# Performance work log

Measured on AMD Instinct MI355X. Metric: run time of the kernel, lower is better.

Reference implementation:

```python
import jax, jax.numpy as jnp
import numpy as np

NUM_NODES = 1_000_000
IN_DIM, HID = 128, 256
B = 4096                 # edges per batch (src/pos/neg each B)
N2 = 3 * B               # seed nodes
FAN = 10
N1 = N2 * FAN            # hop-1 nodes
N0 = N1 * FAN            # hop-0 nodes


def setup_inputs() -> dict:
    key = jax.random.key(0)
    ks = jax.random.split(key, 16)
    g = lambda k, shp, scale: jax.random.normal(k, shp, dtype=jnp.float32) * scale
    return {
        "node_feat": g(ks[0], (NUM_NODES, IN_DIM), 1.0),
        "gids0": jax.random.randint(ks[1], (N0,), 0, NUM_NODES, dtype=jnp.int32),
        "neigh_idx0": jax.random.randint(ks[2], (N1, FAN), 0, N0, dtype=jnp.int32),
        "neigh_idx1": jax.random.randint(ks[3], (N2, FAN), 0, N1, dtype=jnp.int32),
        "W_self0": g(ks[4], (IN_DIM, HID), (1.0 / IN_DIM) ** 0.5),
        "W_neigh0": g(ks[5], (IN_DIM, HID), (1.0 / IN_DIM) ** 0.5),
        "b0": jnp.zeros((HID,), jnp.float32),
        "W_self1": g(ks[6], (HID, HID), (1.0 / HID) ** 0.5),
        "W_neigh1": g(ks[7], (HID, HID), (1.0 / HID) ** 0.5),
        "b1": jnp.zeros((HID,), jnp.float32),
        "Wp1": g(ks[8], (HID, HID), (1.0 / HID) ** 0.5),
        "bp1": jnp.zeros((HID,), jnp.float32),
        "Wp2": g(ks[9], (HID, HID), (1.0 / HID) ** 0.5),
        "bp2": jnp.zeros((HID,), jnp.float32),
        "Wp3": g(ks[10], (HID, 1), (1.0 / HID) ** 0.5),
        "bp3": jnp.zeros((1,), jnp.float32),
    }


def _sage(x, n_dst, neigh, Ws, Wn, b):
    # x: [n_src, d]; neigh: [n_dst, fan] local indices into x
    x_dst = x[:n_dst]                       # dst nodes are a prefix of src nodes
    agg = jnp.mean(x[neigh], axis=1)        # [n_dst, d] mean aggregation
    return x_dst @ Ws + agg @ Wn + b


def reference(node_feat, gids0, neigh_idx0, neigh_idx1,
              W_self0, W_neigh0, b0, W_self1, W_neigh1, b1,
              Wp1, bp1, Wp2, bp2, Wp3, bp3):
    # embedding gather for the full sampled neighborhood
    x = node_feat[gids0]                                    # [N0, IN_DIM]
    h = jax.nn.relu(_sage(x, N1, neigh_idx0, W_self0, W_neigh0, b0))  # [N1, HID]
    h = _sage(h, N2, neigh_idx1, W_self1, W_neigh1, b1)     # [N2, HID]
    src, pos, neg = h[:B], h[B:2 * B], h[2 * B:3 * B]
    # predictor on elementwise product of endpoint embeddings
    z = jnp.concatenate([src, src], axis=0) * jnp.concatenate([pos, neg], axis=0)
    z = jax.nn.relu(z @ Wp1 + bp1)
    z = jax.nn.relu(z @ Wp2 + bp2)
    scores = z @ Wp3 + bp3                                  # [2B, 1]
    return scores
```

## Files before the change

kernel.cpp:

```cpp
#include <hip/hip_runtime.h>
#include <hip/hip_bf16.h>

#define NNODES 1000000
#define INDIM  128
#define HIDC   256
#define BSZ    4096
#define N2C    12288
#define FANC   10
#define N1C    122880
#define N0C    1228800

typedef __bf16 bf16_t;
typedef bf16_t bf16x2 __attribute__((ext_vector_type(2)));
typedef bf16_t bf16x4 __attribute__((ext_vector_type(4)));
typedef bf16_t bf16x8 __attribute__((ext_vector_type(8)));
typedef float  f32x4  __attribute__((ext_vector_type(4)));

__global__ __launch_bounds__(256) void prep_w(const float* __restrict__ SA,
                                              const float* __restrict__ SB,
                                              bf16_t* __restrict__ dst,
                                              int Khalf, int Ktot, int N) {
  int t = blockIdx.x * 256 + threadIdx.x;
  if (t >= N * Ktot) return;
  int n = t / Ktot, k = t - n * Ktot;
  float v = (k < Khalf) ? SA[(size_t)k * N + n] : SB[(size_t)(k - Khalf) * N + n];
  dst[t] = (bf16_t)v;
}

__global__ __launch_bounds__(256) void gather0(const float* __restrict__ feat,
                                               const int* __restrict__ gids,
                                               const int* __restrict__ nidx,
                                               bf16_t* __restrict__ A0) {
  int wv = (blockIdx.x * 256 + threadIdx.x) >> 6;
  int d = __builtin_amdgcn_readfirstlane(wv);
  int lane = threadIdx.x & 63;
  const float2* f2 = (const float2*)feat;
  int idx[FANC];
#pragma unroll
  for (int j = 0; j < FANC; j++) idx[j] = nidx[d * FANC + j];
  int nid[FANC];
#pragma unroll
  for (int j = 0; j < FANC; j++) nid[j] = gids[idx[j]];
  float ax = 0.f, ay = 0.f;
#pragma unroll
  for (int j = 0; j < FANC; j++) {
    float2 v = f2[(size_t)nid[j] * 64 + lane];
    ax += v.x; ay += v.y;
  }
  int sn = gids[d];
  float2 xs = f2[(size_t)sn * 64 + lane];
  bf16_t* row = A0 + (size_t)d * 256;
  bf16x2 w0 = { (bf16_t)xs.x, (bf16_t)xs.y };
  *(bf16x2*)(row + lane * 2) = w0;
  bf16x2 w1 = { (bf16_t)(ax * 0.1f), (bf16_t)(ay * 0.1f) };
  *(bf16x2*)(row + 128 + lane * 2) = w1;
}

__global__ __launch_bounds__(256) void gather1(const bf16_t* __restrict__ h,
                                               const int* __restrict__ nidx,
                                               bf16_t* __restrict__ A1) {
  int wv = (blockIdx.x * 256 + threadIdx.x) >> 6;
  int d = __builtin_amdgcn_readfirstlane(wv);
  int lane = threadIdx.x & 63;
  const bf16x4* h4 = (const bf16x4*)h;
  int idx[FANC];
#pragma unroll
  for (int j = 0; j < FANC; j++) idx[j] = nidx[d * FANC + j];
  float a0 = 0.f, a1 = 0.f, a2 = 0.f, a3 = 0.f;
#pragma unroll
  for (int j = 0; j < FANC; j++) {
    bf16x4 v = h4[(size_t)idx[j] * 64 + lane];
    a0 += (float)v[0]; a1 += (float)v[1]; a2 += (float)v[2]; a3 += (float)v[3];
  }
  bf16x4 xs = h4[(size_t)d * 64 + lane];
  bf16x4* out = (bf16x4*)(A1 + (size_t)d * 512);
  out[lane] = xs;
  bf16x4 ag = { (bf16_t)(a0 * 0.1f), (bf16_t)(a1 * 0.1f),
                (bf16_t)(a2 * 0.1f), (bf16_t)(a3 * 0.1f) };
  out[64 + lane] = ag;
}

template<int K, int MT, bool RELU, bool OUTBF>
__global__ __launch_bounds__(256) void gemm_mfma(const bf16_t* __restrict__ A,
                                                 const bf16_t* __restrict__ Wt,
                                                 const float* __restrict__ bias,
                                                 void* __restrict__ Cout) {
  int tid = threadIdx.x;
  int wv = tid >> 6, lane = tid & 63;
  int l15 = lane & 15, quad = lane >> 4;
  int m0 = blockIdx.x * (MT * 16);
  int n0 = wv * 64;
  f32x4 acc[MT][4] = {};
  for (int k0 = 0; k0 < K; k0 += 32) {
    bf16x8 a[MT], b[4];
#pragma unroll
    for (int mt = 0; mt < MT; mt++)
      a[mt] = *(const bf16x8*)(A + (size_t)(m0 + mt * 16 + l15) * K + k0 + quad * 8);
#pragma unroll
    for (int nt = 0; nt < 4; nt++)
      b[nt] = *(const bf16x8*)(Wt + (size_t)(n0 + nt * 16 + l15) * K + k0 + quad * 8);
#pragma unroll
    for (int mt = 0; mt < MT; mt++)
#pragma unroll
      for (int nt = 0; nt < 4; nt++)
        acc[mt][nt] = __builtin_amdgcn_mfma_f32_16x16x32_bf16(a[mt], b[nt], acc[mt][nt], 0, 0, 0);
  }
#pragma unroll
  for (int mt = 0; mt < MT; mt++) {
#pragma unroll
    for (int nt = 0; nt < 4; nt++) {
      int col = n0 + nt * 16 + l15;
      float bv = bias[col];
#pragma unroll
      for (int r = 0; r < 4; r++) {
        int row = m0 + mt * 16 + quad * 4 + r;
        float v = acc[mt][nt][r] + bv;
        if (RELU) v = fmaxf(v, 0.f);
        if (OUTBF) ((bf16_t*)Cout)[(size_t)row * 256 + col] = (bf16_t)v;
        else       ((float*)Cout)[(size_t)row * 256 + col] = v;
      }
    }
  }
}

__global__ __launch_bounds__(256) void zbuild(const float* __restrict__ h2,
                                              bf16_t* __restrict__ z) {
  int t = blockIdx.x * 256 + threadIdx.x;
  int r = t >> 6, c = (t & 63) * 4;
  int a = r & 4095, b = r + 4096;
  float4 va = *(const float4*)(h2 + (size_t)a * 256 + c);
  float4 vb = *(const float4*)(h2 + (size_t)b * 256 + c);
  bf16x4 o = { (bf16_t)(va.x * vb.x), (bf16_t)(va.y * vb.y),
               (bf16_t)(va.z * vb.z), (bf16_t)(va.w * vb.w) };
  *(bf16x4*)(z + (size_t)r * 256 + c) = o;
}

__global__ __launch_bounds__(256) void pred3(const bf16_t* __restrict__ z2,
                                             const float* __restrict__ Wp3,
                                             const float* __restrict__ bp3,
                                             float* __restrict__ out) {
  int wv = (blockIdx.x * 256 + threadIdx.x) >> 6;
  int lane = threadIdx.x & 63;
  bf16x4 v = ((const bf16x4*)z2)[(size_t)wv * 64 + lane];
  float4 w = ((const float4*)Wp3)[lane];
  float s = (float)v[0] * w.x + (float)v[1] * w.y + (float)v[2] * w.z + (float)v[3] * w.w;
  for (int off = 32; off > 0; off >>= 1) s += __shfl_down(s, off);
  if (lane == 0) out[wv] = s + bp3[0];
}

extern "C" void kernel_launch(void* const* d_in, const int* in_sizes, int n_in,
                              void* d_out, int out_size, void* d_ws, size_t ws_size,
                              hipStream_t stream) {
  const float* node_feat = (const float*)d_in[0];
  const int*   gids0     = (const int*)d_in[1];
  const int*   nidx0     = (const int*)d_in[2];
  const int*   nidx1     = (const int*)d_in[3];
  const float* Wself0    = (const float*)d_in[4];
  const float* Wneigh0   = (const float*)d_in[5];
  const float* b0        = (const float*)d_in[6];
  const float* Wself1    = (const float*)d_in[7];
  const float* Wneigh1   = (const float*)d_in[8];
  const float* b1        = (const float*)d_in[9];
  const float* Wp1       = (const float*)d_in[10];
  const float* bp1       = (const float*)d_in[11];
  const float* Wp2       = (const float*)d_in[12];
  const float* bp2       = (const float*)d_in[13];
  const float* Wp3       = (const float*)d_in[14];
  const float* bp3       = (const float*)d_in[15];

  char* ws = (char*)d_ws;
  bf16_t* Wt0  = (bf16_t*)(ws + 0);
  bf16_t* Wt1  = (bf16_t*)(ws + (128 << 10));
  bf16_t* WtP1 = (bf16_t*)(ws + (384 << 10));
  bf16_t* WtP2 = (bf16_t*)(ws + (512 << 10));
  char* big = ws + (1 << 20);
  bf16_t* A0 = (bf16_t*)big;
  bf16_t* h  = (bf16_t*)(big + 62914560ULL);
  bf16_t* A1 = (bf16_t*)big;
  float*  h2 = (float*)(big + (16ULL << 20));
  bf16_t* z  = (bf16_t*)(big + (32ULL << 20));
  bf16_t* z1 = (bf16_t*)(big + (40ULL << 20));
  bf16_t* z2 = (bf16_t*)(big + (48ULL << 20));
  float* out = (float*)d_out;

  prep_w<<<256, 256, 0, stream>>>(Wself0, Wneigh0, Wt0, INDIM, 256, HIDC);
  prep_w<<<512, 256, 0, stream>>>(Wself1, Wneigh1, Wt1, HIDC, 512, HIDC);
  prep_w<<<256, 256, 0, stream>>>(Wp1, Wp1, WtP1, HIDC, 256, HIDC);
  prep_w<<<256, 256, 0, stream>>>(Wp2, Wp2, WtP2, HIDC, 256, HIDC);

  gather0<<<N1C / 4, 256, 0, stream>>>(node_feat, gids0, nidx0, A0);
  gemm_mfma<256, 4, true, true><<<N1C / 64, 256, 0, stream>>>(A0, Wt0, b0, h);

  gather1<<<N2C / 4, 256, 0, stream>>>(h, nidx1, A1);
  gemm_mfma<512, 2, false, false><<<N2C / 32, 256, 0, stream>>>(A1, Wt1, b1, h2);

  zbuild<<<2048, 256, 0, stream>>>(h2, z);
  gemm_mfma<256, 2, true, true><<<8192 / 32, 256, 0, stream>>>(z,  WtP1, bp1, z1);
  gemm_mfma<256, 2, true, true><<<8192 / 32, 256, 0, stream>>>(z1, WtP2, bp2, z2);
  pred3<<<2048, 256, 0, stream>>>(z2, Wp3, bp3, out);
}
```

Measured before the change: 830.9 us.

## Fuse neighbor gather with SAGE GEMMs via LDS-staged A tiles

Merges each gather kernel with its following MFMA GEMM. A block gathers its 64 (or 32) destination rows (self feature plus mean of neighbors) into padded shared memory, then runs the GEMM directly from LDS. This removes the global write and re-read of the A0/A1 intermediates and two launches. In exchange each block serializes gather then compute, LDS use limits occupancy, and each wave handles 16 rows sequentially, so gather latency may be less well hidden.

```diff
diff --git a/kernel.cpp b/kernel.cpp
--- a/kernel.cpp
+++ b/kernel.cpp
@@ -27,57 +27,141 @@
   dst[t] = (bf16_t)v;
 }
 
-__global__ __launch_bounds__(256) void gather0(const float* __restrict__ feat,
-                                               const int* __restrict__ gids,
-                                               const int* __restrict__ nidx,
-                                               bf16_t* __restrict__ A0) {
-  int wv = (blockIdx.x * 256 + threadIdx.x) >> 6;
-  int d = __builtin_amdgcn_readfirstlane(wv);
-  int lane = threadIdx.x & 63;
+#define LDA0 264
+__global__ __launch_bounds__(256) void fused0(const float* __restrict__ feat,
+                                              const int* __restrict__ gids,
+                                              const int* __restrict__ nidx,
+                                              const bf16_t* __restrict__ Wt,
+                                              const float* __restrict__ bias,
+                                              bf16_t* __restrict__ h) {
+  __shared__ __align__(16) bf16_t As[64 * LDA0];
+  __shared__ int nid_s[64 * FANC];
+  __shared__ int self_s[64];
+  int tid = threadIdx.x;
+  int m0 = blockIdx.x * 64;
+
+  for (int t = tid; t < 64 * FANC; t += 256)
+    nid_s[t] = gids[nidx[(size_t)m0 * FANC + t]];
+  if (tid < 64) self_s[tid] = gids[m0 + tid];
+  __syncthreads();
+
+  int wv = tid >> 6, lane = tid & 63;
   const float2* f2 = (const float2*)feat;
-  int idx[FANC];
-#pragma unroll
-  for (int j = 0; j < FANC; j++) idx[j] = nidx[d * FANC + j];
-  int nid[FANC];
-#pragma unroll
-  for (int j = 0; j < FANC; j++) nid[j] = gids[idx[j]];
-  float ax = 0.f, ay = 0.f;
-#pragma unroll
-  for (int j = 0; j < FANC; j++) {
-    float2 v = f2[(size_t)nid[j] * 64 + lane];
-    ax += v.x; ay += v.y;
-  }
-  int sn = gids[d];
-  float2 xs = f2[(size_t)sn * 64 + lane];
-  bf16_t* row = A0 + (size_t)d * 256;
-  bf16x2 w0 = { (bf16_t)xs.x, (bf16_t)xs.y };
-  *(bf16x2*)(row + lane * 2) = w0;
-  bf16x2 w1 = { (bf16_t)(ax * 0.1f), (bf16_t)(ay * 0.1f) };
-  *(bf16x2*)(row + 128 + lane * 2) = w1;
-}
-
-__global__ __launch_bounds__(256) void gather1(const bf16_t* __restrict__ h,
-                                               const int* __restrict__ nidx,
-                                               bf16_t* __restrict__ A1) {
-  int wv = (blockIdx.x * 256 + threadIdx.x) >> 6;
-  int d = __builtin_amdgcn_readfirstlane(wv);
-  int lane = threadIdx.x & 63;
+  for (int i = 0; i < 16; i++) {
+    int d = wv * 16 + i;
+    float ax = 0.f, ay = 0.f;
+#pragma unroll
+    for (int j = 0; j < FANC; j++) {
+      int nd = nid_s[d * FANC + j];
+      float2 v = f2[(size_t)nd * 64 + lane];
+      ax += v.x; ay += v.y;
+    }
+    int sn = self_s[d];
+    float2 xs = f2[(size_t)sn * 64 + lane];
+    bf16_t* row = As + d * LDA0;
+    bf16x2 w0 = { (bf16_t)xs.x, (bf16_t)xs.y };
+    *(bf16x2*)(row + lane * 2) = w0;
+    bf16x2 w1 = { (bf16_t)(ax * 0.1f), (bf16_t)(ay * 0.1f) };
+    *(bf16x2*)(row + 128 + lane * 2) = w1;
+  }
+  __syncthreads();
+
+  int l15 = lane & 15, quad = lane >> 4;
+  int n0 = wv * 64;
+  f32x4 acc[4][4] = {};
+  for (int k0 = 0; k0 < 256; k0 += 32) {
+    bf16x8 a[4], b[4];
+#pragma unroll
+    for (int mt = 0; mt < 4; mt++)
+      a[mt] = *(const bf16x8*)(As + (mt * 16 + l15) * LDA0 + k0 + quad * 8);
+#pragma unroll
+    for (int nt = 0; nt < 4; nt++)
+      b[nt] = *(const bf16x8*)(Wt + (size_t)(n0 + nt * 16 + l15) * 256 + k0 + quad * 8);
+#pragma unroll
+    for (int mt = 0; mt < 4; mt++)
+#pragma unroll
+      for (int nt = 0; nt < 4; nt++)
+        acc[mt][nt] = __builtin_amdgcn_mfma_f32_16x16x32_bf16(a[mt], b[nt], acc[mt][nt], 0, 0, 0);
+  }
+#pragma unroll
+  for (int mt = 0; mt < 4; mt++)
+#pragma unroll
+    for (int nt = 0; nt < 4; nt++) {
+      int col = n0 + nt * 16 + l15;
+      float bv = bias[col];
+#pragma unroll
+      for (int r = 0; r < 4; r++) {
+        int row = m0 + mt * 16 + quad * 4 + r;
+        float v = fmaxf(acc[mt][nt][r] + bv, 0.f);
+        h[(size_t)row * 256 + col] = (bf16_t)v;
+      }
+    }
+}
+
+#define LDA1 520
+__global__ __launch_bounds__(256) void fused1(const bf16_t* __restrict__ h,
+                                              const int* __restrict__ nidx,
+                                              const bf16_t* __restrict__ Wt,
+                                              const float* __restrict__ bias,
+                                              float* __restrict__ h2) {
+  __shared__ __align__(16) bf16_t As[32 * LDA1];
+  __shared__ int nid_s[32 * FANC];
+  int tid = threadIdx.x;
+  int m0 = blockIdx.x * 32;
+
+  for (int t = tid; t < 32 * FANC; t += 256)
+    nid_s[t] = nidx[(size_t)m0 * FANC + t];
+  __syncthreads();
+
+  int wv = tid >> 6, lane = tid & 63;
   const bf16x4* h4 = (const bf16x4*)h;
-  int idx[FANC];
-#pragma unroll
-  for (int j = 0; j < FANC; j++) idx[j] = nidx[d * FANC + j];
-  float a0 = 0.f, a1 = 0.f, a2 = 0.f, a3 = 0.f;
-#pragma unroll
-  for (int j = 0; j < FANC; j++) {
-    bf16x4 v = h4[(size_t)idx[j] * 64 + lane];
-    a0 += (float)v[0]; a1 += (float)v[1]; a2 += (float)v[2]; a3 += (float)v[3];
-  }
-  bf16x4 xs = h4[(size_t)d * 64 + lane];
-  bf16x4* out = (bf16x4*)(A1 + (size_t)d * 512);
-  out[lane] = xs;
-  bf16x4 ag = { (bf16_t)(a0 * 0.1f), (bf16_t)(a1 * 0.1f),
-                (bf16_t)(a2 * 0.1f), (bf16_t)(a3 * 0.1f) };
-  out[64 + lane] = ag;
+  for (int i = 0; i < 8; i++) {
+    int d = wv * 8 + i;
+    float a0 = 0.f, a1 = 0.f, a2 = 0.f, a3 = 0.f;
+#pragma unroll
+    for (int j = 0; j < FANC; j++) {
+      int nd = nid_s[d * FANC + j];
+      bf16x4 v = h4[(size_t)nd * 64 + lane];
+      a0 += (float)v[0]; a1 += (float)v[1]; a2 += (float)v[2]; a3 += (float)v[3];
+    }
+    bf16x4 xs = h4[(size_t)(m0 + d) * 64 + lane];
+    bf16_t* row = As + d * LDA1;
+    *(bf16x4*)(row + lane * 4) = xs;
+    bf16x4 ag = { (bf16_t)(a0 * 0.1f), (bf16_t)(a1 * 0.1f),
+                  (bf16_t)(a2 * 0.1f), (bf16_t)(a3 * 0.1f) };
+    *(bf16x4*)(row + 256 + lane * 4) = ag;
+  }
+  __syncthreads();
+
+  int l15 = lane & 15, quad = lane >> 4;
+  int n0 = wv * 64;
+  f32x4 acc[2][4] = {};
+  for (int k0 = 0; k0 < 512; k0 += 32) {
+    bf16x8 a[2], b[4];
+#pragma unroll
+    for (int mt = 0; mt < 2; mt++)
+      a[mt] = *(const bf16x8*)(As + (mt * 16 + l15) * LDA1 + k0 + quad * 8);
+#pragma unroll
+    for (int nt = 0; nt < 4; nt++)
+      b[nt] = *(const bf16x8*)(Wt + (size_t)(n0 + nt * 16 + l15) * 512 + k0 + quad * 8);
+#pragma unroll
+    for (int mt = 0; mt < 2; mt++)
+#pragma unroll
+      for (int nt = 0; nt < 4; nt++)
+        acc[mt][nt] = __builtin_amdgcn_mfma_f32_16x16x32_bf16(a[mt], b[nt], acc[mt][nt], 0, 0, 0);
+  }
+#pragma unroll
+  for (int mt = 0; mt < 2; mt++)
+#pragma unroll
+    for (int nt = 0; nt < 4; nt++) {
+      int col = n0 + nt * 16 + l15;
+      float bv = bias[col];
+#pragma unroll
+      for (int r = 0; r < 4; r++) {
+        int row = m0 + mt * 16 + quad * 4 + r;
+        h2[(size_t)row * 256 + col] = acc[mt][nt][r] + bv;
+      }
+    }
 }
 
 template<int K, int MT, bool RELU, bool OUTBF>
@@ -106,7 +190,7 @@
         acc[mt][nt] = __builtin_amdgcn_mfma_f32_16x16x32_bf16(a[mt], b[nt], acc[mt][nt], 0, 0, 0);
   }
 #pragma unroll
-  for (int mt = 0; mt < MT; mt++) {
+  for (int mt = 0; mt < MT; mt++)
 #pragma unroll
     for (int nt = 0; nt < 4; nt++) {
       int col = n0 + nt * 16 + l15;
@@ -120,7 +204,6 @@
         else       ((float*)Cout)[(size_t)row * 256 + col] = v;
       }
     }
-  }
 }
 
 __global__ __launch_bounds__(256) void zbuild(const float* __restrict__ h2,
@@ -174,13 +257,11 @@
   bf16_t* WtP1 = (bf16_t*)(ws + (384 << 10));
   bf16_t* WtP2 = (bf16_t*)(ws + (512 << 10));
   char* big = ws + (1 << 20);
-  bf16_t* A0 = (bf16_t*)big;
-  bf16_t* h  = (bf16_t*)(big + 62914560ULL);
-  bf16_t* A1 = (bf16_t*)big;
-  float*  h2 = (float*)(big + (16ULL << 20));
-  bf16_t* z  = (bf16_t*)(big + (32ULL << 20));
-  bf16_t* z1 = (bf16_t*)(big + (40ULL << 20));
-  bf16_t* z2 = (bf16_t*)(big + (48ULL << 20));
+  bf16_t* h  = (bf16_t*)big;
+  float*  h2 = (float*)(big + (64ULL << 20));
+  bf16_t* z  = (bf16_t*)(big + (80ULL << 20));
+  bf16_t* z1 = (bf16_t*)(big + (88ULL << 20));
+  bf16_t* z2 = (bf16_t*)(big + (96ULL << 20));
   float* out = (float*)d_out;
 
   prep_w<<<256, 256, 0, stream>>>(Wself0, Wneigh0, Wt0, INDIM, 256, HIDC);
@@ -188,11 +269,9 @@
   prep_w<<<256, 256, 0, stream>>>(Wp1, Wp1, WtP1, HIDC, 256, HIDC);
   prep_w<<<256, 256, 0, stream>>>(Wp2, Wp2, WtP2, HIDC, 256, HIDC);
 
-  gather0<<<N1C / 4, 256, 0, stream>>>(node_feat, gids0, nidx0, A0);
-  gemm_mfma<256, 4, true, true><<<N1C / 64, 256, 0, stream>>>(A0, Wt0, b0, h);
-
-  gather1<<<N2C / 4, 256, 0, stream>>>(h, nidx1, A1);
-  gemm_mfma<512, 2, false, false><<<N2C / 32, 256, 0, stream>>>(A1, Wt1, b1, h2);
+  fused0<<<N1C / 64, 256, 0, stream>>>(node_feat, gids0, nidx0, Wt0, b0, h);
+
+  fused1<<<N2C / 32, 256, 0, stream>>>(h, nidx1, Wt1, b1, h2);
 
   zbuild<<<2048, 256, 0, stream>>>(h2, z);
   gemm_mfma<256, 2, true, true><<<8192 / 32, 256, 0, stream>>>(z,  WtP1, bp1, z1);
```

After: 781.7 us. 1.06x faster.
